# Kernel optimization log

Measured on AMD Instinct MI355X. Metric: run time of the kernel, lower is better.

Reference implementation:

```python
import jax, jax.numpy as jnp
import numpy as np

B, S, D = 8, 1024, 1024
H, DK = 16, 64  # heads, key_size (== head_size)
NEG = 1e12


def setup_inputs() -> dict:
    key = jax.random.key(0)
    ks = jax.random.split(key, 10)
    s = 1.0 / np.sqrt(D)
    return {
        "q": jax.random.normal(ks[0], (B, S, D), jnp.float32),
        "k": jax.random.normal(ks[1], (B, S, D), jnp.float32),
        "v": jax.random.normal(ks[2], (B, S, D), jnp.float32),
        "pos_bias": jax.random.normal(ks[3], (S, S, DK), jnp.float32) * 0.02,
        "Wq": jax.random.normal(ks[4], (D, H * DK), jnp.float32) * s,
        "Wk": jax.random.normal(ks[5], (D, H * DK), jnp.float32) * s,
        "Wv": jax.random.normal(ks[6], (D, H * DK), jnp.float32) * s,
        "Wo": jax.random.normal(ks[7], (H * DK, D), jnp.float32) * s,
        "bq": jnp.zeros((H * DK,), jnp.float32),
        "bk": jnp.zeros((H * DK,), jnp.float32),
        "bv": jnp.zeros((H * DK,), jnp.float32),
        "bo": jnp.zeros((D,), jnp.float32),
        "q_mask": jnp.ones((B, S), jnp.int32),
        "v_mask": jnp.ones((B, S), jnp.int32),
    }


def reference(q, k, v, pos_bias, Wq, Wk, Wv, Wo, bq, bk, bv, bo, q_mask, v_mask):
    qm = q_mask.astype(q.dtype)  # [B,Sq]
    vm = v_mask.astype(q.dtype)  # [B,Sk]
    # Projections (faithful quirk: K is projected from v, as in the source)
    qw = (q @ Wq + bq).reshape(B, S, H, DK)
    kw = (v @ Wk + bk).reshape(B, S, H, DK)
    vw = (v @ Wv + bv).reshape(B, S, H, DK)
    # scores + inline relative-position bias ('typial_relative' branch)
    a = jnp.einsum('bjhd,bkhd->bhjk', qw, kw)
    a = a + jnp.einsum('bjhd,jkd->bhjk', qw, pos_bias)
    a = a / jnp.sqrt(jnp.asarray(DK, a.dtype))
    # additive key mask, then softmax over keys
    a = a - (1.0 - vm)[:, None, None, :] * NEG
    a = jax.nn.softmax(a, axis=-1)
    o = jnp.einsum('bhjk,bkhd->bjhd', a, vw)  # [B,Sq,H,DK]
    o = o.reshape(B, S, H * DK) @ Wo + bo
    # multiplicative query mask on output
    o = o * qm[:, :, None]
    return o
```

## Files before the change

kernel.cpp:

```cpp
#include <hip/hip_runtime.h>

using short8 = __attribute__((ext_vector_type(8))) short;
using f32x4  = __attribute__((ext_vector_type(4))) float;
using u16x4  = __attribute__((ext_vector_type(4))) unsigned short;
using fl4    = __attribute__((ext_vector_type(4))) float;

#define MFMA16(a, b, c) __builtin_amdgcn_mfma_f32_16x16x32_bf16((a), (b), (c), 0, 0, 0)

static __device__ __forceinline__ unsigned short f2bf(float f) {
  union { float f; unsigned u; } x; x.f = f;
  return (unsigned short)((x.u + 0x7FFFu + ((x.u >> 16) & 1u)) >> 16);
}
static __device__ __forceinline__ float bf2f(unsigned short s) {
  union { unsigned u; float f; } x; x.u = ((unsigned)s) << 16;
  return x.f;
}
static __device__ __forceinline__ float fexp2(float x) {
  float r; asm("v_exp_f32 %0, %1" : "=v"(r) : "v"(x)); return r;
}
static __device__ __forceinline__ unsigned pk2(float lo, float hi) {
  unsigned r; asm("v_cvt_pk_bf16_f32 %0, %1, %2" : "=v"(r) : "v"(lo), "v"(hi));
  return r;
}

static __device__ __forceinline__ void gload16(const void* g, void* l) {
  __builtin_amdgcn_global_load_lds((const __attribute__((address_space(1))) void*)g,
                                   (__attribute__((address_space(3))) void*)l, 16, 0, 0);
}

#define LOG2E 1.4426950408889634f

__global__ __launch_bounds__(256) void k_wconv4(
    const float* __restrict__ W0, const float* __restrict__ W1,
    const float* __restrict__ W2, const float* __restrict__ W3,
    unsigned short* __restrict__ Wt0, unsigned short* __restrict__ Wt1,
    unsigned short* __restrict__ Wt2, unsigned short* __restrict__ Wt3) {
  const float* W = (blockIdx.z == 0) ? W0 : (blockIdx.z == 1) ? W1
                   : (blockIdx.z == 2) ? W2 : W3;
  unsigned short* Wt = (blockIdx.z == 0) ? Wt0 : (blockIdx.z == 1) ? Wt1
                       : (blockIdx.z == 2) ? Wt2 : Wt3;
  __shared__ float tile[64][65];
  const int t = threadIdx.x;
  const int n0 = blockIdx.x * 64, k0 = blockIdx.y * 64;
#pragma unroll
  for (int p = 0; p < 4; ++p) {
    int row = p * 16 + (t >> 4);
    int c4 = (t & 15) * 4;
    fl4 val = *(const fl4*)&W[(size_t)(k0 + row) * 1024 + n0 + c4];
    tile[row][c4 + 0] = val[0];
    tile[row][c4 + 1] = val[1];
    tile[row][c4 + 2] = val[2];
    tile[row][c4 + 3] = val[3];
  }
  __syncthreads();
#pragma unroll
  for (int p = 0; p < 4; ++p) {
    int n = p * 16 + (t >> 4);
    int k4 = (t & 15) * 4;
    u16x4 u;
    u[0] = f2bf(tile[k4 + 0][n]);
    u[1] = f2bf(tile[k4 + 1][n]);
    u[2] = f2bf(tile[k4 + 2][n]);
    u[3] = f2bf(tile[k4 + 3][n]);
    *(u16x4*)&Wt[(size_t)(n0 + n) * 1024 + k0 + k4] = u;
  }
}

__global__ __launch_bounds__(256) void k_cvt(const float* __restrict__ a,
                                             const float* __restrict__ b,
                                             unsigned short* __restrict__ oa,
                                             unsigned short* __restrict__ ob) {
  const float* src = blockIdx.y ? b : a;
  unsigned short* dst = blockIdx.y ? ob : oa;
  size_t i = ((size_t)blockIdx.x * 256 + threadIdx.x) * 8;
  fl4 v0 = *(const fl4*)&src[i];
  fl4 v1 = *(const fl4*)&src[i + 4];
  u16x4 u0, u1;
  u0[0] = f2bf(v0[0]); u0[1] = f2bf(v0[1]); u0[2] = f2bf(v0[2]); u0[3] = f2bf(v0[3]);
  u1[0] = f2bf(v1[0]); u1[1] = f2bf(v1[1]); u1[2] = f2bf(v1[2]); u1[3] = f2bf(v1[3]);
  *(u16x4*)&dst[i] = u0;
  *(u16x4*)&dst[i + 4] = u1;
}

#define GEMM3_CORE(APTR, BPTR)                                                  \
  const int t = threadIdx.x, lane = t & 63, w = t >> 6;                         \
  const int g = lane >> 4, ln = lane & 15;                                      \
  const int wm = w >> 1, wn = w & 1;                                            \
  __shared__ unsigned short sh[24576];    \
  const int srow = lane >> 2;                                                   \
  const int sc = (lane & 3) ^ ((lane >> 3) & 3);                                \
  const int rsw = ((ln >> 1) & 3);                                              \
  f32x4 acc[4][4] = {};                                                         \
  _Pragma("unroll") for (int pre = 0; pre < 2; ++pre) {                         \
    _Pragma("unroll") for (int p = 0; p < 2; ++p) {                             \
      gload16(&APTR[(size_t)(m0 + p * 64 + w * 16 + srow) * 1024 + pre * 32 + sc * 8], \
              &sh[pre * 8192 + (p * 64 + w * 16) * 32]);                        \
      gload16(&BPTR[(size_t)(n0 + p * 64 + w * 16 + srow) * 1024 + pre * 32 + sc * 8], \
              &sh[pre * 8192 + 4096 + (p * 64 + w * 16) * 32]);                 \
    }                                                                           \
  }                                                                             \
  int cur = 0;                                                                  \
  for (int tt = 0; tt < 32; ++tt) {                                             \
    if (tt < 31) {                                                              \
      asm volatile("s_waitcnt vmcnt(4)" ::: "memory");                          \
    } else {                                                                    \
      asm volatile("s_waitcnt vmcnt(0)" ::: "memory");                          \
    }                                                                           \
    __builtin_amdgcn_sched_barrier(0);                                          \
    __builtin_amdgcn_s_barrier();                                               \
    __builtin_amdgcn_sched_barrier(0);                                          \
    if (tt < 30) {                                                              \
      int bb = cur + 2; if (bb >= 3) bb -= 3;                                   \
      int kk = (tt + 2) * 32;                                                   \
      _Pragma("unroll") for (int p = 0; p < 2; ++p) {                           \
        gload16(&APTR[(size_t)(m0 + p * 64 + w * 16 + srow) * 1024 + kk + sc * 8], \
                &sh[bb * 8192 + (p * 64 + w * 16) * 32]);                       \
        gload16(&BPTR[(size_t)(n0 + p * 64 + w * 16 + srow) * 1024 + kk + sc * 8], \
                &sh[bb * 8192 + 4096 + (p * 64 + w * 16) * 32]);                \
      }                                                                         \
    }                                                                           \
    const unsigned short* As = &sh[cur * 8192];                                 \
    const unsigned short* Bs = As + 4096;                                       \
    short8 af[4], bfr[4];                                                       \
    _Pragma("unroll") for (int fm = 0; fm < 4; ++fm)                            \
        af[fm] = *(const short8*)&As[(wm * 64 + fm * 16 + ln) * 32 + (g ^ rsw) * 8]; \
    _Pragma("unroll") for (int fn = 0; fn < 4; ++fn)                            \
        bfr[fn] = *(const short8*)&Bs[(wn * 64 + fn * 16 + ln) * 32 + (g ^ rsw) * 8]; \
    _Pragma("unroll") for (int fn = 0; fn < 4; ++fn) {                          \
      _Pragma("unroll") for (int fm = 0; fm < 4; ++fm)                          \
          acc[fm][fn] = MFMA16(af[fm], bfr[fn], acc[fm][fn]);                   \
    }                                                                           \
    cur = (cur == 2) ? 0 : cur + 1;                                             \
  }

__global__ __launch_bounds__(256) void k_proj3(
    const unsigned short* __restrict__ QB, const unsigned short* __restrict__ VB,
    const unsigned short* __restrict__ WtQ, const unsigned short* __restrict__ WtK,
    const unsigned short* __restrict__ WtV,
    const float* __restrict__ bq, const float* __restrict__ bk,
    const float* __restrict__ bv,
    unsigned short* __restrict__ QW, unsigned short* __restrict__ KW,
    unsigned short* __restrict__ VWT) {
  const int mode = blockIdx.z;
  const unsigned short* A8 = (mode == 0) ? QB : VB;
  const unsigned short* Wt = (mode == 0) ? WtQ : (mode == 1) ? WtK : WtV;
  const float* bias = (mode == 0) ? bq : (mode == 1) ? bk : bv;
  const int n0 = blockIdx.x * 128, m0 = blockIdx.y * 128;
  GEMM3_CORE(A8, Wt)
  __syncthreads();
  const float scale = (mode == 0) ? (0.125f * LOG2E) : 1.0f;
#pragma unroll
  for (int fn = 0; fn < 4; ++fn) {
    float bn = bias[n0 + wn * 64 + fn * 16 + ln];
#pragma unroll
    for (int fm = 0; fm < 4; ++fm) {
#pragma unroll
      for (int r = 0; r < 4; ++r) {
        float val = (acc[fm][fn][r] + bn) * scale;
        sh[(wm * 64 + fm * 16 + 4 * g + r) * 132 + wn * 64 + fn * 16 + ln] = f2bf(val);
      }
    }
  }
  __syncthreads();
  if (mode < 2) {
    unsigned short* OUT = (mode == 0) ? QW : KW;
#pragma unroll
    for (int p = 0; p < 16; ++p) {
      int row = p * 8 + (t >> 5), c4 = (t & 31) * 4;
      *(u16x4*)&OUT[(size_t)(m0 + row) * 1024 + n0 + c4] =
          *(const u16x4*)&sh[row * 132 + c4];
    }
  } else {
    const int b = m0 >> 10, s0 = m0 & 1023;
#pragma unroll
    for (int p = 0; p < 16; ++p) {
#pragma unroll
      for (int qh = 0; qh < 2; ++qh) {
        int hdl = p * 8 + (t >> 5);
        int sl = qh * 64 + (t & 31) * 2;
        unsigned lo = sh[sl * 132 + hdl];
        unsigned hi = sh[(sl + 1) * 132 + hdl];
        int hd = n0 + hdl;
        int h = hd >> 6, d = hd & 63;
        *(unsigned*)&VWT[((size_t)(b * 16 + h) * 64 + d) * 1024 + s0 + sl] =
            lo | (hi << 16);
      }
    }
  }
}

__global__ __launch_bounds__(256) void k_out3(
    const unsigned short* __restrict__ OB, const unsigned short* __restrict__ WtO,
    const float* __restrict__ bo, const int* __restrict__ qmask,
    float* __restrict__ out) {
  const int n0 = blockIdx.x * 128, m0 = blockIdx.y * 128;
  GEMM3_CORE(OB, WtO)
  float bn[4];
#pragma unroll
  for (int fn = 0; fn < 4; ++fn) bn[fn] = bo[n0 + wn * 64 + fn * 16 + ln];
#pragma unroll
  for (int fm = 0; fm < 4; ++fm) {
#pragma unroll
    for (int r = 0; r < 4; ++r) {
      int row = m0 + wm * 64 + fm * 16 + 4 * g + r;
      float qm = (float)qmask[row];
#pragma unroll
      for (int fn = 0; fn < 4; ++fn)
        out[(size_t)row * 1024 + n0 + wn * 64 + fn * 16 + ln] =
            (acc[fm][fn][r] + bn[fn]) * qm;
    }
  }
}

__global__ __launch_bounds__(256) void k_pbias(
    const unsigned short* __restrict__ QW, const float* __restrict__ pb,
    const int* __restrict__ vmask, unsigned short* __restrict__ CB, int jbase) {
  const int kt = blockIdx.x;
  const int jl = blockIdx.y;
  const int j = jbase + jl;
  const int t = threadIdx.x, lane = t & 63, w = t >> 6;
  const int g = lane >> 4, ln = lane & 15;
  const int wm = w >> 1, wn = w & 1;
  __shared__ unsigned short sm[18432];
  unsigned short* a_lds = sm;
  unsigned short* b_lds = sm + 9216;
#pragma unroll
  for (int p = 0; p < 8; ++p) {
    int i4 = p * 256 + t;
    int row = i4 >> 4, c4 = (i4 & 15) * 4;
    *(u16x4*)&a_lds[row * 72 + c4] =
        *(const u16x4*)&QW[((size_t)(row >> 4) * 1024 + j) * 1024 + (row & 15) * 64 + c4];
  }
#pragma unroll
  for (int p = 0; p < 8; ++p) {
    int i4 = p * 256 + t;
    int row = i4 >> 4, c4 = (i4 & 15) * 4;
    fl4 val = *(const fl4*)&pb[((size_t)j * 1024 + kt * 128 + row) * 64 + c4];
    u16x4 u;
    u[0] = f2bf(val[0]); u[1] = f2bf(val[1]);
    u[2] = f2bf(val[2]); u[3] = f2bf(val[3]);
    *(u16x4*)&b_lds[row * 72 + c4] = u;
  }
  __syncthreads();
  f32x4 acc[4][4] = {};
#pragma unroll
  for (int ks = 0; ks < 2; ++ks) {
    short8 af[4];
#pragma unroll
    for (int fm = 0; fm < 4; ++fm)
      af[fm] = *(const short8*)&a_lds[(wm * 64 + fm * 16 + ln) * 72 + ks * 32 + 8 * g];
#pragma unroll
    for (int fn = 0; fn < 4; ++fn) {
      short8 bfr = *(const short8*)&b_lds[(wn * 64 + fn * 16 + ln) * 72 + ks * 32 + 8 * g];
#pragma unroll
      for (int fm = 0; fm < 4; ++fm) acc[fm][fn] = MFMA16(af[fm], bfr, acc[fm][fn]);
    }
  }
  __syncthreads();
#pragma unroll
  for (int fn = 0; fn < 4; ++fn) {
    int kcol = kt * 128 + wn * 64 + fn * 16 + ln;
#pragma unroll
    for (int fm = 0; fm < 4; ++fm) {
      float off = vmask[(wm * 4 + fm) * 1024 + kcol] ? 0.f : (-1e12f * LOG2E);
#pragma unroll
      for (int r = 0; r < 4; ++r)
        sm[(wm * 64 + fm * 16 + 4 * g + r) * 132 + wn * 64 + fn * 16 + ln] =
            f2bf(acc[fm][fn][r] + off);
    }
  }
  __syncthreads();
#pragma unroll
  for (int p = 0; p < 16; ++p) {
    int row = p * 8 + (t >> 5), c4 = (t & 31) * 4;
    *(u16x4*)&CB[((size_t)row * 512 + jl) * 1024 + kt * 128 + c4] =
        *(const u16x4*)&sm[row * 132 + c4];
  }
}

__global__ __launch_bounds__(256) void k_attn(
    const unsigned short* __restrict__ QW, const unsigned short* __restrict__ KW,
    const unsigned short* __restrict__ VWT, const unsigned short* __restrict__ CB,
    unsigned short* __restrict__ OB, int jbase) {
  const int B = blockIdx.x;
  const int wrk = (B & 7) * 128 + (B >> 3);
  const int jt = wrk & 7, h = (wrk >> 3) & 15, b = wrk >> 7;
  const int t = threadIdx.x, lane = t & 63, w = t >> 6;
  const int g = lane >> 4, ln = lane & 15;
  const int j0 = jbase + jt * 64;
  const int jl0 = jt * 64;
  __shared__ unsigned short lds_kv[2][16384];
  short8 qf[2];
  {
    const size_t qrow = ((size_t)b * 1024 + (j0 + w * 16 + ln)) * 1024 + h * 64;
    qf[0] = *(const short8*)&QW[qrow + 8 * g];
    qf[1] = *(const short8*)&QW[qrow + 32 + 8 * g];
  }
  const size_t cb_row = ((size_t)(b * 16 + h) * 512 + jl0 + w * 16 + ln) * 1024;

  const int kc = (lane & 7) ^ ((lane >> 3) & 7);
  const int vrow_l = (w << 2) + (lane >> 4);
  const int vc = (lane & 15) ^ vrow_l;
  const int krk = ln & 7;
  const int vrk = ln;

#define STAGE(kt_, bi)                                                            \
  {                                                                               \
    _Pragma("unroll") for (int r = 0; r < 4; ++r) {                               \
      gload16(&KW[((size_t)b * 1024 + (kt_) * 128 + r * 32 + w * 8 + (lane >> 3)) * 1024 + \
                  h * 64 + kc * 8],                                               \
              &lds_kv[bi][r * 2048 + w * 512 + lane * 8]);                        \
      gload16(&VWT[((size_t)(b * 16 + h) * 64 + r * 16 + vrow_l) * 1024 +         \
                   (kt_) * 128 + vc * 8],                                         \
              &lds_kv[bi][8192 + r * 2048 + w * 512 + lane * 8]);                 \
    }                                                                             \
  }

  u16x4 rcb[8];
  STAGE(0, 0);
  __builtin_amdgcn_sched_barrier(0);
#pragma unroll
  for (int p = 0; p < 8; ++p)
    rcb[p] = *(const u16x4*)&CB[cb_row + p * 16 + 4 * g];
  __builtin_amdgcn_sched_barrier(0);
  STAGE(1, 1);
  __builtin_amdgcn_sched_barrier(0);

  f32x4 o_acc[4] = {};
  float l_par = 0.f;

  for (int kt = 0; kt < 8; ++kt) {
    if (kt == 0) {
      asm volatile("s_waitcnt vmcnt(16)" ::: "memory");
    } else {
      asm volatile("s_waitcnt vmcnt(8)" ::: "memory");
    }
    __builtin_amdgcn_sched_barrier(0);
    __builtin_amdgcn_s_barrier();
    __builtin_amdgcn_sched_barrier(0);
    if (kt >= 1 && kt < 7) STAGE(kt + 1, (kt + 1) & 1);
    __builtin_amdgcn_sched_barrier(0);
    f32x4 s[8];
#pragma unroll
    for (int fm = 0; fm < 8; ++fm) {
#pragma unroll
      for (int r = 0; r < 4; ++r) s[fm][r] = bf2f(rcb[fm][r]);
    }
    if (kt < 7) {
#pragma unroll
      for (int p = 0; p < 8; ++p)
        rcb[p] = *(const u16x4*)&CB[cb_row + (kt + 1) * 128 + p * 16 + 4 * g];
    }
    __builtin_amdgcn_sched_barrier(0);
    const unsigned short* Kb = lds_kv[kt & 1];
    const unsigned short* Vb = Kb + 8192;
    __builtin_amdgcn_s_setprio(1);
#pragma unroll
    for (int ks = 0; ks < 2; ++ks) {
#pragma unroll
      for (int fm = 0; fm < 8; ++fm) {
        short8 af = *(const short8*)&Kb[(fm * 16 + ln) * 64 + (((ks * 4 + g) ^ krk) * 8)];
        s[fm] = MFMA16(af, qf[ks], s[fm]);
      }
    }
    __builtin_amdgcn_s_setprio(0);
#pragma unroll
    for (int ks = 0; ks < 4; ++ks) {
      const int fA = 2 * ks, fB = 2 * ks + 1;
      float eA0 = fexp2(s[fA][0] - 17.0f), eA1 = fexp2(s[fA][1] - 17.0f);
      float eA2 = fexp2(s[fA][2] - 17.0f), eA3 = fexp2(s[fA][3] - 17.0f);
      float eB0 = fexp2(s[fB][0] - 17.0f), eB1 = fexp2(s[fB][1] - 17.0f);
      float eB2 = fexp2(s[fB][2] - 17.0f), eB3 = fexp2(s[fB][3] - 17.0f);
      l_par += ((eA0 + eA1) + (eA2 + eA3)) + ((eB0 + eB1) + (eB2 + eB3));
      unsigned a0 = pk2(eA0, eA1), a1 = pk2(eA2, eA3);
      unsigned b0 = pk2(eB0, eB1), b1 = pk2(eB2, eB3);
      asm("v_permlane32_swap_b32 %0, %1" : "+v"(a0), "+v"(b0));
      asm("v_permlane16_swap_b32 %0, %1" : "+v"(a0), "+v"(b0));
      asm("v_permlane32_swap_b32 %0, %1" : "+v"(a1), "+v"(b1));
      asm("v_permlane16_swap_b32 %0, %1" : "+v"(a1), "+v"(b1));
      union { short8 v; unsigned u[4]; } bp;
      bp.u[0] = a0; bp.u[1] = a1; bp.u[2] = b0; bp.u[3] = b1;
      __builtin_amdgcn_s_setprio(1);
#pragma unroll
      for (int fm = 0; fm < 4; ++fm) {
        short8 av = *(const short8*)&Vb[(fm * 16 + ln) * 128 + (((ks * 4 + g) ^ vrk) * 8)];
        o_acc[fm] = MFMA16(av, bp.v, o_acc[fm]);
      }
      __builtin_amdgcn_s_setprio(0);
    }
  }
  l_par += __shfl_xor(l_par, 16);
  l_par += __shfl_xor(l_par, 32);
  float inv = 1.0f / l_par;
  const size_t orow = ((size_t)b * 1024 + (j0 + w * 16 + ln)) * 1024 + h * 64;
#pragma unroll
  for (int fm = 0; fm < 4; ++fm) {
    union { u16x4 v; unsigned u[2]; } uo;
    uo.u[0] = pk2(o_acc[fm][0] * inv, o_acc[fm][1] * inv);
    uo.u[1] = pk2(o_acc[fm][2] * inv, o_acc[fm][3] * inv);
    *(u16x4*)&OB[orow + fm * 16 + 4 * g] = uo.v;
  }
#undef STAGE
}

extern "C" void kernel_launch(void* const* d_in, const int* in_sizes, int n_in,
                              void* d_out, int out_size, void* d_ws, size_t ws_size,
                              hipStream_t stream) {
  const float* q  = (const float*)d_in[0];
  const float* v  = (const float*)d_in[2];
  const float* pb = (const float*)d_in[3];
  const float* Wq = (const float*)d_in[4];
  const float* Wk = (const float*)d_in[5];
  const float* Wv = (const float*)d_in[6];
  const float* Wo = (const float*)d_in[7];
  const float* bq = (const float*)d_in[8];
  const float* bk = (const float*)d_in[9];
  const float* bv = (const float*)d_in[10];
  const float* bo = (const float*)d_in[11];
  const int* qm = (const int*)d_in[12];
  const int* vm = (const int*)d_in[13];
  float* out = (float*)d_out;

  unsigned short* ws = (unsigned short*)d_ws;
  const size_t M1 = 1024 * 1024;
  unsigned short* WTQ = ws;
  unsigned short* WTK = WTQ + M1;
  unsigned short* WTV = WTK + M1;
  unsigned short* WTO = WTV + M1;
  unsigned short* QB  = WTO + M1;
  unsigned short* VB  = QB + 8 * M1;
  unsigned short* QW  = VB + 8 * M1;
  unsigned short* KW  = QW + 8 * M1;
  unsigned short* VWT = KW + 8 * M1;
  unsigned short* OB  = VWT + 8 * M1;
  unsigned short* CB  = OB + 8 * M1;

  k_wconv4<<<dim3(16, 16, 4), 256, 0, stream>>>(Wq, Wk, Wv, Wo, WTQ, WTK, WTV, WTO);
  k_cvt<<<dim3(4096, 2), 256, 0, stream>>>(q, v, QB, VB);
  k_proj3<<<dim3(8, 64, 3), 256, 0, stream>>>(QB, VB, WTQ, WTK, WTV, bq, bk, bv,
                                              QW, KW, VWT);
  for (int st = 0; st < 2; ++st) {
    k_pbias<<<dim3(8, 512), 256, 0, stream>>>(QW, pb, vm, CB, st * 512);
    k_attn<<<dim3(1024), 256, 0, stream>>>(QW, KW, VWT, CB, OB, st * 512);
  }
  k_out3<<<dim3(8, 64), 256, 0, stream>>>(OB, WTO, bo, qm, out);
}
```

Before: 364.8 us.

## Switch attention kernel to 32x32 MFMA tiles with 32 query rows per wave

The attention kernel now uses 32x32x16 bf16 MFMA instead of 16x16x32, so each wave owns 32 query rows instead of 16. Each block covers 128 queries and the grid shrinks from 1024 to 512 blocks. Every K/V tile staged in LDS is therefore reused by twice as many queries, and the softmax permlane shuffle becomes a single swap per pair. The cost is higher register pressure (larger accumulators and bias prefetch buffers) and fewer blocks, which could lower occupancy and parallelism on a 256-CU device.

```diff
diff --git a/kernel.cpp b/kernel.cpp
--- a/kernel.cpp
+++ b/kernel.cpp
@@ -2,10 +2,12 @@
 
 using short8 = __attribute__((ext_vector_type(8))) short;
 using f32x4  = __attribute__((ext_vector_type(4))) float;
+using f32x16 = __attribute__((ext_vector_type(16))) float;
 using u16x4  = __attribute__((ext_vector_type(4))) unsigned short;
 using fl4    = __attribute__((ext_vector_type(4))) float;
 
 #define MFMA16(a, b, c) __builtin_amdgcn_mfma_f32_16x16x32_bf16((a), (b), (c), 0, 0, 0)
+#define MFMA32(a, b, c) __builtin_amdgcn_mfma_f32_32x32x16_bf16((a), (b), (c), 0, 0, 0)
 
 static __device__ __forceinline__ unsigned short f2bf(float f) {
   union { float f; unsigned u; } x; x.f = f;
@@ -283,26 +285,27 @@
     const unsigned short* __restrict__ VWT, const unsigned short* __restrict__ CB,
     unsigned short* __restrict__ OB, int jbase) {
   const int B = blockIdx.x;
-  const int wrk = (B & 7) * 128 + (B >> 3);
-  const int jt = wrk & 7, h = (wrk >> 3) & 15, b = wrk >> 7;
+  const int wrk = (B & 7) * 64 + (B >> 3);
+  const int jt = wrk & 3, h = (wrk >> 2) & 15, b = wrk >> 6;
   const int t = threadIdx.x, lane = t & 63, w = t >> 6;
-  const int g = lane >> 4, ln = lane & 15;
-  const int j0 = jbase + jt * 64;
-  const int jl0 = jt * 64;
+  const int l31 = lane & 31, hf = lane >> 5;
+  const int j0 = jbase + jt * 128 + w * 32;
+  const int jl0 = jt * 128 + w * 32;
   __shared__ unsigned short lds_kv[2][16384];
-  short8 qf[2];
+  short8 qf[4];
   {
-    const size_t qrow = ((size_t)b * 1024 + (j0 + w * 16 + ln)) * 1024 + h * 64;
-    qf[0] = *(const short8*)&QW[qrow + 8 * g];
-    qf[1] = *(const short8*)&QW[qrow + 32 + 8 * g];
-  }
-  const size_t cb_row = ((size_t)(b * 16 + h) * 512 + jl0 + w * 16 + ln) * 1024;
+    const size_t qrow = ((size_t)b * 1024 + (j0 + l31)) * 1024 + h * 64;
+#pragma unroll
+    for (int ds = 0; ds < 4; ++ds)
+      qf[ds] = *(const short8*)&QW[qrow + ds * 16 + 8 * hf];
+  }
+  const size_t cb_row = ((size_t)(b * 16 + h) * 512 + jl0 + l31) * 1024;
 
   const int kc = (lane & 7) ^ ((lane >> 3) & 7);
   const int vrow_l = (w << 2) + (lane >> 4);
   const int vc = (lane & 15) ^ vrow_l;
-  const int krk = ln & 7;
-  const int vrk = ln;
+  const int krk = l31 & 7;
+  const int vrk = l31 & 15;
 
 #define STAGE(kt_, bi)                                                            \
   {                                                                               \
@@ -316,91 +319,100 @@
     }                                                                             \
   }
 
-  u16x4 rcb[8];
+  u16x4 rcb[16];
+#define LOAD_CB(kt_)                                                              \
+  {                                                                               \
+    _Pragma("unroll") for (int kf = 0; kf < 4; ++kf) {                            \
+      _Pragma("unroll") for (int q = 0; q < 4; ++q)                               \
+          rcb[kf * 4 + q] = *(const u16x4*)&CB[cb_row + (kt_) * 128 + kf * 32 +   \
+                                               q * 8 + 4 * hf];                   \
+    }                                                                             \
+  }
+
   STAGE(0, 0);
   __builtin_amdgcn_sched_barrier(0);
-#pragma unroll
-  for (int p = 0; p < 8; ++p)
-    rcb[p] = *(const u16x4*)&CB[cb_row + p * 16 + 4 * g];
+  LOAD_CB(0);
   __builtin_amdgcn_sched_barrier(0);
   STAGE(1, 1);
   __builtin_amdgcn_sched_barrier(0);
 
-  f32x4 o_acc[4] = {};
+  f32x16 o_acc[2] = {};
   float l_par = 0.f;
 
   for (int kt = 0; kt < 8; ++kt) {
     if (kt == 0) {
+      asm volatile("s_waitcnt vmcnt(24)" ::: "memory");
+    } else {
       asm volatile("s_waitcnt vmcnt(16)" ::: "memory");
-    } else {
-      asm volatile("s_waitcnt vmcnt(8)" ::: "memory");
     }
     __builtin_amdgcn_sched_barrier(0);
     __builtin_amdgcn_s_barrier();
     __builtin_amdgcn_sched_barrier(0);
     if (kt >= 1 && kt < 7) STAGE(kt + 1, (kt + 1) & 1);
     __builtin_amdgcn_sched_barrier(0);
-    f32x4 s[8];
-#pragma unroll
-    for (int fm = 0; fm < 8; ++fm) {
-#pragma unroll
-      for (int r = 0; r < 4; ++r) s[fm][r] = bf2f(rcb[fm][r]);
-    }
-    if (kt < 7) {
-#pragma unroll
-      for (int p = 0; p < 8; ++p)
-        rcb[p] = *(const u16x4*)&CB[cb_row + (kt + 1) * 128 + p * 16 + 4 * g];
-    }
+    f32x16 st[4];
+#pragma unroll
+    for (int kf = 0; kf < 4; ++kf) {
+#pragma unroll
+      for (int q = 0; q < 4; ++q) {
+#pragma unroll
+        for (int r = 0; r < 4; ++r) st[kf][q * 4 + r] = bf2f(rcb[kf * 4 + q][r]);
+      }
+    }
+    if (kt < 7) LOAD_CB(kt + 1);
     __builtin_amdgcn_sched_barrier(0);
     const unsigned short* Kb = lds_kv[kt & 1];
     const unsigned short* Vb = Kb + 8192;
     __builtin_amdgcn_s_setprio(1);
 #pragma unroll
-    for (int ks = 0; ks < 2; ++ks) {
-#pragma unroll
-      for (int fm = 0; fm < 8; ++fm) {
-        short8 af = *(const short8*)&Kb[(fm * 16 + ln) * 64 + (((ks * 4 + g) ^ krk) * 8)];
-        s[fm] = MFMA16(af, qf[ks], s[fm]);
+    for (int ds = 0; ds < 4; ++ds) {
+#pragma unroll
+      for (int kf = 0; kf < 4; ++kf) {
+        short8 af =
+            *(const short8*)&Kb[(kf * 32 + l31) * 64 + (((ds * 2 + hf) ^ krk) * 8)];
+        st[kf] = MFMA32(af, qf[ds], st[kf]);
       }
     }
     __builtin_amdgcn_s_setprio(0);
 #pragma unroll
-    for (int ks = 0; ks < 4; ++ks) {
-      const int fA = 2 * ks, fB = 2 * ks + 1;
-      float eA0 = fexp2(s[fA][0] - 17.0f), eA1 = fexp2(s[fA][1] - 17.0f);
-      float eA2 = fexp2(s[fA][2] - 17.0f), eA3 = fexp2(s[fA][3] - 17.0f);
-      float eB0 = fexp2(s[fB][0] - 17.0f), eB1 = fexp2(s[fB][1] - 17.0f);
-      float eB2 = fexp2(s[fB][2] - 17.0f), eB3 = fexp2(s[fB][3] - 17.0f);
-      l_par += ((eA0 + eA1) + (eA2 + eA3)) + ((eB0 + eB1) + (eB2 + eB3));
-      unsigned a0 = pk2(eA0, eA1), a1 = pk2(eA2, eA3);
-      unsigned b0 = pk2(eB0, eB1), b1 = pk2(eB2, eB3);
-      asm("v_permlane32_swap_b32 %0, %1" : "+v"(a0), "+v"(b0));
-      asm("v_permlane16_swap_b32 %0, %1" : "+v"(a0), "+v"(b0));
-      asm("v_permlane32_swap_b32 %0, %1" : "+v"(a1), "+v"(b1));
-      asm("v_permlane16_swap_b32 %0, %1" : "+v"(a1), "+v"(b1));
+    for (int ks = 0; ks < 8; ++ks) {
+      const int kf = ks >> 1, bs = (ks & 1) * 8;
+      float e0 = fexp2(st[kf][bs + 0] - 17.0f), e1 = fexp2(st[kf][bs + 1] - 17.0f);
+      float e2 = fexp2(st[kf][bs + 2] - 17.0f), e3 = fexp2(st[kf][bs + 3] - 17.0f);
+      float e4 = fexp2(st[kf][bs + 4] - 17.0f), e5 = fexp2(st[kf][bs + 5] - 17.0f);
+      float e6 = fexp2(st[kf][bs + 6] - 17.0f), e7 = fexp2(st[kf][bs + 7] - 17.0f);
+      l_par += ((e0 + e1) + (e2 + e3)) + ((e4 + e5) + (e6 + e7));
+      unsigned A0 = pk2(e0, e1), A1 = pk2(e2, e3);
+      unsigned C0 = pk2(e4, e5), C1 = pk2(e6, e7);
+      asm("v_permlane32_swap_b32 %0, %1" : "+v"(A0), "+v"(C0));
+      asm("v_permlane32_swap_b32 %0, %1" : "+v"(A1), "+v"(C1));
       union { short8 v; unsigned u[4]; } bp;
-      bp.u[0] = a0; bp.u[1] = a1; bp.u[2] = b0; bp.u[3] = b1;
+      bp.u[0] = A0; bp.u[1] = A1; bp.u[2] = C0; bp.u[3] = C1;
       __builtin_amdgcn_s_setprio(1);
 #pragma unroll
-      for (int fm = 0; fm < 4; ++fm) {
-        short8 av = *(const short8*)&Vb[(fm * 16 + ln) * 128 + (((ks * 4 + g) ^ vrk) * 8)];
-        o_acc[fm] = MFMA16(av, bp.v, o_acc[fm]);
+      for (int df = 0; df < 2; ++df) {
+        short8 av = *(const short8*)&Vb[(df * 32 + l31) * 128 +
+                                        (((ks * 2 + hf) ^ vrk) * 8)];
+        o_acc[df] = MFMA32(av, bp.v, o_acc[df]);
       }
       __builtin_amdgcn_s_setprio(0);
     }
   }
-  l_par += __shfl_xor(l_par, 16);
   l_par += __shfl_xor(l_par, 32);
   float inv = 1.0f / l_par;
-  const size_t orow = ((size_t)b * 1024 + (j0 + w * 16 + ln)) * 1024 + h * 64;
-#pragma unroll
-  for (int fm = 0; fm < 4; ++fm) {
-    union { u16x4 v; unsigned u[2]; } uo;
-    uo.u[0] = pk2(o_acc[fm][0] * inv, o_acc[fm][1] * inv);
-    uo.u[1] = pk2(o_acc[fm][2] * inv, o_acc[fm][3] * inv);
-    *(u16x4*)&OB[orow + fm * 16 + 4 * g] = uo.v;
+  const size_t orow = ((size_t)b * 1024 + (j0 + l31)) * 1024 + h * 64;
+#pragma unroll
+  for (int df = 0; df < 2; ++df) {
+#pragma unroll
+    for (int q = 0; q < 4; ++q) {
+      union { u16x4 v; unsigned u[2]; } uo;
+      uo.u[0] = pk2(o_acc[df][q * 4 + 0] * inv, o_acc[df][q * 4 + 1] * inv);
+      uo.u[1] = pk2(o_acc[df][q * 4 + 2] * inv, o_acc[df][q * 4 + 3] * inv);
+      *(u16x4*)&OB[orow + df * 32 + q * 8 + 4 * hf] = uo.v;
+    }
   }
 #undef STAGE
+#undef LOAD_CB
 }
 
 extern "C" void kernel_launch(void* const* d_in, const int* in_sizes, int n_in,
@@ -441,7 +453,7 @@
                                               QW, KW, VWT);
   for (int st = 0; st < 2; ++st) {
     k_pbias<<<dim3(8, 512), 256, 0, stream>>>(QW, pb, vm, CB, st * 512);
-    k_attn<<<dim3(1024), 256, 0, stream>>>(QW, KW, VWT, CB, OB, st * 512);
+    k_attn<<<dim3(512), 256, 0, stream>>>(QW, KW, VWT, CB, OB, st * 512);
   }
   k_out3<<<dim3(8, 64), 256, 0, stream>>>(OB, WTO, bo, qm, out);
 }
```

Result: no change. 358.2 us (-1.8%).
